# Optimization experiments

Hardware: AMD Instinct MI355X
Metric: run time of the kernel (lower is better)

## Reference

```python
import jax, jax.numpy as jnp
import numpy as np

N, C, H, W = 1024, 16, 32, 32
E = 4096


def setup_inputs() -> dict:
    key = jax.random.key(0)
    ks = jax.random.split(key, 10)
    feats = jax.random.normal(ks[0], (N, C, H, W), dtype=jnp.float32)
    src = jax.random.randint(ks[1], (E,), 0, N)
    dst = jax.random.randint(ks[2], (E,), 0, N)
    sign = jax.random.randint(ks[3], (E,), 0, 2) * 2 - 1  # values in {-1, +1}
    edges = jnp.stack([src, sign, dst], axis=1).astype(jnp.int64)
    s = 0.05
    w1 = jax.random.normal(ks[4], (2 * C, 3 * C, 3, 3), dtype=jnp.float32) * s
    b1 = jnp.zeros((2 * C,), dtype=jnp.float32)
    w2 = jax.random.normal(ks[5], (2 * C, 2 * C, 3, 3), dtype=jnp.float32) * s
    b2 = jnp.zeros((2 * C,), dtype=jnp.float32)
    w3 = jax.random.normal(ks[6], (C, 2 * C, 3, 3), dtype=jnp.float32) * s
    b3 = jnp.zeros((C,), dtype=jnp.float32)
    return {"feats": feats, "edges": edges, "w1": w1, "b1": b1,
            "w2": w2, "b2": b2, "w3": w3, "b3": b3}


def _pool_edges(edges, feats, positive):
    # Bidirectional gather + scatter_add over selected edges.
    # Mask-by-zero keeps shapes static (equivalent math to torch.where selection).
    sign = edges[:, 1]
    mask = (sign > 0) if positive else (sign < 0)
    w = mask.astype(feats.dtype)[:, None, None, None]
    src = edges[:, 0]
    dst = edges[:, 2]
    pooled = jnp.zeros_like(feats)
    pooled = pooled.at[dst].add(feats[src] * w)  # src -> dst
    pooled = pooled.at[src].add(feats[dst] * w)  # dst -> src
    return pooled


def _conv(x, w, b):
    y = jax.lax.conv_general_dilated(
        x, w, window_strides=(1, 1), padding=((1, 1), (1, 1)),
        dimension_numbers=("NCHW", "OIHW", "NCHW"))
    return y + b[None, :, None, None]


def _leaky(x):
    return jax.nn.leaky_relu(x, negative_slope=0.1)


def reference(feats, edges, w1, b1, w2, b2, w3, b3):
    pos = _pool_edges(edges, feats, positive=True)
    neg = _pool_edges(edges, feats, positive=False)
    x = jnp.concatenate([feats, pos, neg], axis=1)  # [N, 3C, H, W]
    x = _leaky(_conv(x, w1, b1))
    x = _leaky(_conv(x, w2, b2))
    x = _leaky(_conv(x, w3, b3))
    return x
```

## Files before the change

### kernel.cpp

```cpp
#include <hip/hip_runtime.h>


#define NIMG 1024
#define CHW  16384
#define NEDGE 4096
#define MAXD 64

#define ICP1 56
#define KP1  456
#define ICP2 40
#define KP2  296
#define XSZ (34*34*ICP1)
#define WSZ (32*KP1)

typedef __attribute__((ext_vector_type(8))) _Float16 half8;
typedef __attribute__((ext_vector_type(4))) _Float16 half4;
typedef __attribute__((ext_vector_type(4))) float float4v;

__device__ __forceinline__ float leaky(float x) { return x > 0.f ? x : 0.1f * x; }

__global__ __launch_bounds__(256) void build_adj(
    const int* __restrict__ edges, int* __restrict__ deg, int* __restrict__ adj)
{
    const int e = blockIdx.x * 256 + threadIdx.x;
    const bool is64 = (edges[1] == 0);
    int s, sg, d;
    if (is64) { s = edges[6*e]; sg = edges[6*e + 2]; d = edges[6*e + 4]; }
    else      { s = edges[3*e]; sg = edges[3*e + 1]; d = edges[3*e + 2]; }
    const int tag_d = (d << 1) | (int)(sg > 0);
    const int tag_s = (s << 1) | (int)(sg > 0);
    int i = atomicAdd(&deg[s], 1); if (i < MAXD) adj[(s << 6) + i] = tag_d;
    int j = atomicAdd(&deg[d], 1); if (j < MAXD) adj[(d << 6) + j] = tag_s;
}

__global__ __launch_bounds__(256) void transpose_kernel(
    const float* __restrict__ feats, _Float16* __restrict__ fcl)
{
    const int n = blockIdx.x, tid = threadIdx.x;
    const float* fb = feats + (size_t)n * CHW;
    _Float16*    ob = fcl   + (size_t)n * 1024 * 16;
    #pragma unroll
    for (int it = 0; it < 4; ++it) {
        int p = it*256 + tid;
        float t[16];
        #pragma unroll
        for (int c = 0; c < 16; ++c) t[c] = fb[(c << 10) + p];
        half8 v0, v1;
        #pragma unroll
        for (int c = 0; c < 8; ++c) { v0[c] = (_Float16)t[c]; v1[c] = (_Float16)t[c+8]; }
        *(half8*)(ob + p*16)     = v0;
        *(half8*)(ob + p*16 + 8) = v1;
    }
}

__global__ __launch_bounds__(1024, 4) void conv_kernel(
    const _Float16* __restrict__ fcl,
    const int* __restrict__ deg, const int* __restrict__ adj,
    const float* __restrict__ w1, const float* __restrict__ b1,
    const float* __restrict__ w2, const float* __restrict__ b2,
    const float* __restrict__ w3, const float* __restrict__ b3,
    float* __restrict__ out)
{
    __shared__ __align__(16) _Float16 Xs[XSZ];
    __shared__ __align__(16) _Float16 Ws[WSZ];
    const int n    = blockIdx.x;
    const int tid  = threadIdx.x;
    const int wave = tid >> 6;
    const int lane = tid & 63;
    const int col  = lane & 15;
    const int quad = lane >> 4;

    {
        const half8* fc = (const half8*)(fcl + (size_t)n * CHW);
        const int p = tid;
        const int base = (((p >> 5) + 1)*34 + (p & 31) + 1) * ICP1;
        *(half8*)(Xs + base)     = fc[2*p];
        *(half8*)(Xs + base + 8) = fc[2*p + 1];

        int m = deg[n]; if (m > MAXD) m = MAXD;
        const int* al = adj + (n << 6);
        float ap[16], an[16];
        #pragma unroll
        for (int c = 0; c < 16; ++c) { ap[c] = 0.f; an[c] = 0.f; }
        for (int i = 0; i < m; ++i) {
            const int v = al[i];
            const half8* fb = (const half8*)(fcl + (size_t)(v >> 1) * CHW);
            half8 x0 = fb[2*p], x1 = fb[2*p + 1];
            if (v & 1) {
                #pragma unroll
                for (int c = 0; c < 8; ++c) { ap[c] += (float)x0[c]; ap[c+8] += (float)x1[c]; }
            } else {
                #pragma unroll
                for (int c = 0; c < 8; ++c) { an[c] += (float)x0[c]; an[c+8] += (float)x1[c]; }
            }
        }
        half8 h0, h1, h2, h3;
        #pragma unroll
        for (int c = 0; c < 8; ++c) { h0[c] = (_Float16)ap[c]; h1[c] = (_Float16)ap[c+8];
                                      h2[c] = (_Float16)an[c]; h3[c] = (_Float16)an[c+8]; }
        *(half8*)(Xs + base + 16) = h0;
        *(half8*)(Xs + base + 24) = h1;
        *(half8*)(Xs + base + 32) = h2;
        *(half8*)(Xs + base + 40) = h3;

        for (int i = tid; i < 32*432; i += 1024) {
            int oc = i / 432, r = i - oc*432;
            int ic = r / 9,   tap = r - ic*9;
            Ws[oc*KP1 + tap*48 + ic] = (_Float16)w1[i];
        }
        if (tid < 132) {
            int hp, wp;
            if      (tid < 34)  { hp = 0;        wp = tid; }
            else if (tid < 68)  { hp = 33;       wp = tid - 34; }
            else if (tid < 100) { hp = tid - 67; wp = 0; }
            else                { hp = tid - 99; wp = 33; }
            int hb = (hp*34 + wp) * ICP1;
            #pragma unroll
            for (int t = 0; t < 6; ++t) *(half8*)(Xs + hb + t*8) = (half8)0;
        }
        if (tid >= 160 && tid < 192) {
            int wb = (tid - 160)*KP1 + 432;
            #pragma unroll
            for (int t = 0; t < 3; ++t) *(half8*)(Ws + wb + t*8) = (half8)0;
        }
    }
    __syncthreads();

    float4v acc[2][4];

    {
        #pragma unroll
        for (int m = 0; m < 2; ++m)
            #pragma unroll
            for (int j = 0; j < 4; ++j) acc[m][j] = (float4v){0.f,0.f,0.f,0.f};
        int pixb[4];
        #pragma unroll
        for (int j = 0; j < 4; ++j) {
            int p = wave*64 + j*16 + col;
            pixb[j] = ((p >> 5)*34 + (p & 31)) * ICP1;
        }
        const int abase = col * KP1 + quad * 8;
        #pragma unroll
        for (int ks = 0; ks < 14; ++ks) {
            int kq  = ks*32 + quad*8;
            int tap = kq / 48;
            int off = 0;
            if (tap < 9) {
                int ic0 = kq - tap*48;
                int dh = tap / 3, dw = tap - dh*3;
                off = (dh*34 + dw)*ICP1 + ic0;
            }
            half8 a0 = *(const half8*)(Ws + abase + ks*32);
            half8 a1 = *(const half8*)(Ws + 16*KP1 + abase + ks*32);
            #pragma unroll
            for (int j = 0; j < 4; ++j) {
                half8 b = *(const half8*)(Xs + pixb[j] + off);
                acc[0][j] = __builtin_amdgcn_mfma_f32_16x16x32_f16(a0, b, acc[0][j], 0, 0, 0);
                acc[1][j] = __builtin_amdgcn_mfma_f32_16x16x32_f16(a1, b, acc[1][j], 0, 0, 0);
            }
        }
    }
    __syncthreads();

    {
        if (tid < 132) {
            int hp, wp;
            if      (tid < 34)  { hp = 0;        wp = tid; }
            else if (tid < 68)  { hp = 33;       wp = tid - 34; }
            else if (tid < 100) { hp = tid - 67; wp = 0; }
            else                { hp = tid - 99; wp = 33; }
            int hb = (hp*34 + wp) * ICP2;
            #pragma unroll
            for (int t = 0; t < 4; ++t) *(half8*)(Xs + hb + t*8) = (half8)0;
        }
        float bv[2][4];
        #pragma unroll
        for (int m = 0; m < 2; ++m)
            #pragma unroll
            for (int r = 0; r < 4; ++r) bv[m][r] = b1[m*16 + quad*4 + r];
        #pragma unroll
        for (int m = 0; m < 2; ++m)
            #pragma unroll
            for (int j = 0; j < 4; ++j) {
                int p = wave*64 + j*16 + col;
                _Float16* y = Xs + ((((p>>5)+1)*34) + (p&31) + 1)*ICP2 + m*16 + quad*4;
                half4 v;
                #pragma unroll
                for (int r = 0; r < 4; ++r) v[r] = (_Float16)leaky(acc[m][j][r] + bv[m][r]);
                *(half4*)y = v;
            }
        for (int i = tid; i < 32*288; i += 1024) {
            int oc = i / 288, r = i - oc*288;
            int ic = r / 9,   tap = r - ic*9;
            Ws[oc*KP2 + tap*32 + ic] = (_Float16)w2[i];
        }
    }
    __syncthreads();

    {
        #pragma unroll
        for (int m = 0; m < 2; ++m)
            #pragma unroll
            for (int j = 0; j < 4; ++j) acc[m][j] = (float4v){0.f,0.f,0.f,0.f};
        int pixb[4];
        #pragma unroll
        for (int j = 0; j < 4; ++j) {
            int p = wave*64 + j*16 + col;
            pixb[j] = ((p >> 5)*34 + (p & 31)) * ICP2;
        }
        const int abase = col * KP2 + quad * 8;
        #pragma unroll
        for (int ks = 0; ks < 9; ++ks) {
            int kq  = ks*32 + quad*8;
            int tap = kq >> 5, ic0 = kq & 31;
            int dh = tap / 3, dw = tap - dh*3;
            int off = (dh*34 + dw)*ICP2 + ic0;
            half8 a0 = *(const half8*)(Ws + abase + ks*32);
            half8 a1 = *(const half8*)(Ws + 16*KP2 + abase + ks*32);
            #pragma unroll
            for (int j = 0; j < 4; ++j) {
                half8 b = *(const half8*)(Xs + pixb[j] + off);
                acc[0][j] = __builtin_amdgcn_mfma_f32_16x16x32_f16(a0, b, acc[0][j], 0, 0, 0);
                acc[1][j] = __builtin_amdgcn_mfma_f32_16x16x32_f16(a1, b, acc[1][j], 0, 0, 0);
            }
        }
    }
    __syncthreads();

    {
        float bv[2][4];
        #pragma unroll
        for (int m = 0; m < 2; ++m)
            #pragma unroll
            for (int r = 0; r < 4; ++r) bv[m][r] = b2[m*16 + quad*4 + r];
        #pragma unroll
        for (int m = 0; m < 2; ++m)
            #pragma unroll
            for (int j = 0; j < 4; ++j) {
                int p = wave*64 + j*16 + col;
                _Float16* y = Xs + ((((p>>5)+1)*34) + (p&31) + 1)*ICP2 + m*16 + quad*4;
                half4 v;
                #pragma unroll
                for (int r = 0; r < 4; ++r) v[r] = (_Float16)leaky(acc[m][j][r] + bv[m][r]);
                *(half4*)y = v;
            }
        for (int i = tid; i < 16*288; i += 1024) {
            int oc = i / 288, r = i - oc*288;
            int ic = r / 9,   tap = r - ic*9;
            Ws[oc*KP2 + tap*32 + ic] = (_Float16)w3[i];
        }
    }
    __syncthreads();

    {
        float4v a3[4];
        #pragma unroll
        for (int j = 0; j < 4; ++j) a3[j] = (float4v){0.f,0.f,0.f,0.f};
        int pixb[4];
        #pragma unroll
        for (int j = 0; j < 4; ++j) {
            int p = wave*64 + j*16 + col;
            pixb[j] = ((p >> 5)*34 + (p & 31)) * ICP2;
        }
        const int abase = col * KP2 + quad * 8;
        #pragma unroll
        for (int ks = 0; ks < 9; ++ks) {
            int kq  = ks*32 + quad*8;
            int tap = kq >> 5, ic0 = kq & 31;
            int dh = tap / 3, dw = tap - dh*3;
            int off = (dh*34 + dw)*ICP2 + ic0;
            half8 a0 = *(const half8*)(Ws + abase + ks*32);
            #pragma unroll
            for (int j = 0; j < 4; ++j) {
                half8 b = *(const half8*)(Xs + pixb[j] + off);
                a3[j] = __builtin_amdgcn_mfma_f32_16x16x32_f16(a0, b, a3[j], 0, 0, 0);
            }
        }
        float bv[4];
        #pragma unroll
        for (int r = 0; r < 4; ++r) bv[r] = b3[quad*4 + r];
        float* op = out + (size_t)n * CHW;
        #pragma unroll
        for (int j = 0; j < 4; ++j) {
            int p = wave*64 + j*16 + col;
            #pragma unroll
            for (int r = 0; r < 4; ++r)
                op[(quad*4 + r)*1024 + p] = leaky(a3[j][r] + bv[r]);
        }
    }
}

extern "C" void kernel_launch(void* const* d_in, const int* in_sizes, int n_in,
                              void* d_out, int out_size, void* d_ws, size_t ws_size,
                              hipStream_t stream) {
    const float* feats = (const float*)d_in[0];
    const int*   edges = (const int*)  d_in[1];
    const float* w1 = (const float*)d_in[2];
    const float* b1 = (const float*)d_in[3];
    const float* w2 = (const float*)d_in[4];
    const float* b2 = (const float*)d_in[5];
    const float* w3 = (const float*)d_in[6];
    const float* b3 = (const float*)d_in[7];
    float* out = (float*)d_out;

    _Float16* fcl = (_Float16*)d_ws;
    int* deg = (int*)((char*)d_ws + (32u << 20));
    int* adj = deg + NIMG;

    hipMemsetAsync(deg, 0, NIMG * sizeof(int), stream);
    build_adj<<<dim3(NEDGE/256), dim3(256), 0, stream>>>(edges, deg, adj);
    transpose_kernel<<<dim3(NIMG), dim3(256), 0, stream>>>(feats, fcl);
    conv_kernel<<<dim3(NIMG), dim3(1024), 0, stream>>>(fcl, deg, adj,
                                                       w1, b1, w2, b2, w3, b3, out);
}
```

Measured before the change: 251.6 us.

## Pre-pack fp16 conv weights once, vectorize transpose loads, unroll neighbor gather

Conv weights are converted to fp16 and packed into the padded per-tap layout once, inside the edge-building kernel, so each conv block can copy them into shared memory with 16-byte vector loads. This replaces the per-block scalar fp32 loads that used divisions and scattered stores. The transpose kernel now reads float4 vectors per channel. The neighbor aggregation loop is unrolled by four so that several gathers are in flight at once. The costs are extra workspace, more registers in the gather loop, and weight packing serialized into the small build_adj grid.

```diff
diff --git a/kernel.cpp b/kernel.cpp
--- a/kernel.cpp
+++ b/kernel.cpp
@@ -13,6 +13,11 @@
 #define XSZ (34*34*ICP1)
 #define WSZ (32*KP1)
 
+#define WG1N (32*KP1)
+#define WG2N (32*KP2)
+#define WG3N (16*KP2)
+#define WGTOT (WG1N+WG2N+WG3N)
+
 typedef __attribute__((ext_vector_type(8))) _Float16 half8;
 typedef __attribute__((ext_vector_type(4))) _Float16 half4;
 typedef __attribute__((ext_vector_type(4))) float float4v;
@@ -20,7 +25,9 @@
 __device__ __forceinline__ float leaky(float x) { return x > 0.f ? x : 0.1f * x; }
 
 __global__ __launch_bounds__(256) void build_adj(
-    const int* __restrict__ edges, int* __restrict__ deg, int* __restrict__ adj)
+    const int* __restrict__ edges, int* __restrict__ deg, int* __restrict__ adj,
+    const float* __restrict__ w1, const float* __restrict__ w2,
+    const float* __restrict__ w3, _Float16* __restrict__ wg)
 {
     const int e = blockIdx.x * 256 + threadIdx.x;
     const bool is64 = (edges[1] == 0);
@@ -31,6 +38,26 @@
     const int tag_s = (s << 1) | (int)(sg > 0);
     int i = atomicAdd(&deg[s], 1); if (i < MAXD) adj[(s << 6) + i] = tag_d;
     int j = atomicAdd(&deg[d], 1); if (j < MAXD) adj[(d << 6) + j] = tag_s;
+
+    for (int t = e; t < WGTOT; t += NEDGE) {
+        _Float16 val = (_Float16)0.f;
+        if (t < WG1N) {
+            int oc = t / KP1, r = t - oc * KP1;
+            if (r < 432) { int tap = r / 48, ic = r - tap * 48;
+                           val = (_Float16)w1[(oc*48 + ic)*9 + tap]; }
+        } else if (t < WG1N + WG2N) {
+            int u = t - WG1N;
+            int oc = u / KP2, r = u - oc * KP2;
+            if (r < 288) { int tap = r / 32, ic = r - tap * 32;
+                           val = (_Float16)w2[(oc*32 + ic)*9 + tap]; }
+        } else {
+            int u = t - (WG1N + WG2N);
+            int oc = u / KP2, r = u - oc * KP2;
+            if (r < 288) { int tap = r / 32, ic = r - tap * 32;
+                           val = (_Float16)w3[(oc*32 + ic)*9 + tap]; }
+        }
+        wg[t] = val;
+    }
 }
 
 __global__ __launch_bounds__(256) void transpose_kernel(
@@ -39,27 +66,26 @@
     const int n = blockIdx.x, tid = threadIdx.x;
     const float* fb = feats + (size_t)n * CHW;
     _Float16*    ob = fcl   + (size_t)n * 1024 * 16;
+    const int p0 = tid * 4;
+    float4v t[16];
     #pragma unroll
-    for (int it = 0; it < 4; ++it) {
-        int p = it*256 + tid;
-        float t[16];
-        #pragma unroll
-        for (int c = 0; c < 16; ++c) t[c] = fb[(c << 10) + p];
+    for (int c = 0; c < 16; ++c) t[c] = *(const float4v*)(fb + (c << 10) + p0);
+    #pragma unroll
+    for (int u = 0; u < 4; ++u) {
         half8 v0, v1;
         #pragma unroll
-        for (int c = 0; c < 8; ++c) { v0[c] = (_Float16)t[c]; v1[c] = (_Float16)t[c+8]; }
-        *(half8*)(ob + p*16)     = v0;
-        *(half8*)(ob + p*16 + 8) = v1;
+        for (int c = 0; c < 8; ++c) { v0[c] = (_Float16)t[c][u]; v1[c] = (_Float16)t[c+8][u]; }
+        *(half8*)(ob + (p0+u)*16)     = v0;
+        *(half8*)(ob + (p0+u)*16 + 8) = v1;
     }
 }
 
 __global__ __launch_bounds__(1024, 4) void conv_kernel(
     const _Float16* __restrict__ fcl,
     const int* __restrict__ deg, const int* __restrict__ adj,
-    const float* __restrict__ w1, const float* __restrict__ b1,
-    const float* __restrict__ w2, const float* __restrict__ b2,
-    const float* __restrict__ w3, const float* __restrict__ b3,
-    float* __restrict__ out)
+    const _Float16* __restrict__ wg,
+    const float* __restrict__ b1, const float* __restrict__ b2,
+    const float* __restrict__ b3, float* __restrict__ out)
 {
     __shared__ __align__(16) _Float16 Xs[XSZ];
     __shared__ __align__(16) _Float16 Ws[WSZ];
@@ -82,7 +108,27 @@
         float ap[16], an[16];
         #pragma unroll
         for (int c = 0; c < 16; ++c) { ap[c] = 0.f; an[c] = 0.f; }
-        for (int i = 0; i < m; ++i) {
+        int i = 0;
+        for (; i + 4 <= m; i += 4) {
+            int v0 = al[i], v1 = al[i+1], v2 = al[i+2], v3 = al[i+3];
+            const half8* f0 = (const half8*)(fcl + (size_t)(v0 >> 1) * CHW);
+            const half8* f1 = (const half8*)(fcl + (size_t)(v1 >> 1) * CHW);
+            const half8* f2 = (const half8*)(fcl + (size_t)(v2 >> 1) * CHW);
+            const half8* f3 = (const half8*)(fcl + (size_t)(v3 >> 1) * CHW);
+            half8 x00 = f0[2*p], x01 = f0[2*p+1];
+            half8 x10 = f1[2*p], x11 = f1[2*p+1];
+            half8 x20 = f2[2*p], x21 = f2[2*p+1];
+            half8 x30 = f3[2*p], x31 = f3[2*p+1];
+            if (v0 & 1) { for (int c = 0; c < 8; ++c) { ap[c] += (float)x00[c]; ap[c+8] += (float)x01[c]; } }
+            else        { for (int c = 0; c < 8; ++c) { an[c] += (float)x00[c]; an[c+8] += (float)x01[c]; } }
+            if (v1 & 1) { for (int c = 0; c < 8; ++c) { ap[c] += (float)x10[c]; ap[c+8] += (float)x11[c]; } }
+            else        { for (int c = 0; c < 8; ++c) { an[c] += (float)x10[c]; an[c+8] += (float)x11[c]; } }
+            if (v2 & 1) { for (int c = 0; c < 8; ++c) { ap[c] += (float)x20[c]; ap[c+8] += (float)x21[c]; } }
+            else        { for (int c = 0; c < 8; ++c) { an[c] += (float)x20[c]; an[c+8] += (float)x21[c]; } }
+            if (v3 & 1) { for (int c = 0; c < 8; ++c) { ap[c] += (float)x30[c]; ap[c+8] += (float)x31[c]; } }
+            else        { for (int c = 0; c < 8; ++c) { an[c] += (float)x30[c]; an[c+8] += (float)x31[c]; } }
+        }
+        for (; i < m; ++i) {
             const int v = al[i];
             const half8* fb = (const half8*)(fcl + (size_t)(v >> 1) * CHW);
             half8 x0 = fb[2*p], x1 = fb[2*p + 1];
@@ -103,10 +149,10 @@
         *(half8*)(Xs + base + 32) = h2;
         *(half8*)(Xs + base + 40) = h3;
 
-        for (int i = tid; i < 32*432; i += 1024) {
-            int oc = i / 432, r = i - oc*432;
-            int ic = r / 9,   tap = r - ic*9;
-            Ws[oc*KP1 + tap*48 + ic] = (_Float16)w1[i];
+        {
+            const half8* src = (const half8*)wg;
+            half8* dst = (half8*)Ws;
+            for (int t = tid; t < WG1N/8; t += 1024) dst[t] = src[t];
         }
         if (tid < 132) {
             int hp, wp;
@@ -117,11 +163,6 @@
             int hb = (hp*34 + wp) * ICP1;
             #pragma unroll
             for (int t = 0; t < 6; ++t) *(half8*)(Xs + hb + t*8) = (half8)0;
-        }
-        if (tid >= 160 && tid < 192) {
-            int wb = (tid - 160)*KP1 + 432;
-            #pragma unroll
-            for (int t = 0; t < 3; ++t) *(half8*)(Ws + wb + t*8) = (half8)0;
         }
     }
     __syncthreads();
@@ -189,10 +230,10 @@
                 for (int r = 0; r < 4; ++r) v[r] = (_Float16)leaky(acc[m][j][r] + bv[m][r]);
                 *(half4*)y = v;
             }
-        for (int i = tid; i < 32*288; i += 1024) {
-            int oc = i / 288, r = i - oc*288;
-            int ic = r / 9,   tap = r - ic*9;
-            Ws[oc*KP2 + tap*32 + ic] = (_Float16)w2[i];
+        {
+            const half8* src = (const half8*)(wg + WG1N);
+            half8* dst = (half8*)Ws;
+            for (int t = tid; t < WG2N/8; t += 1024) dst[t] = src[t];
         }
     }
     __syncthreads();
@@ -244,10 +285,10 @@
                 for (int r = 0; r < 4; ++r) v[r] = (_Float16)leaky(acc[m][j][r] + bv[m][r]);
                 *(half4*)y = v;
             }
-        for (int i = tid; i < 16*288; i += 1024) {
-            int oc = i / 288, r = i - oc*288;
-            int ic = r / 9,   tap = r - ic*9;
-            Ws[oc*KP2 + tap*32 + ic] = (_Float16)w3[i];
+        {
+            const half8* src = (const half8*)(wg + WG1N + WG2N);
+            half8* dst = (half8*)Ws;
+            for (int t = tid; t < WG3N/8; t += 1024) dst[t] = src[t];
         }
     }
     __syncthreads();
@@ -306,10 +347,11 @@
     _Float16* fcl = (_Float16*)d_ws;
     int* deg = (int*)((char*)d_ws + (32u << 20));
     int* adj = deg + NIMG;
+    _Float16* wg = (_Float16*)((char*)d_ws + (32u << 20) + 4096 + NIMG*MAXD*4);
 
     hipMemsetAsync(deg, 0, NIMG * sizeof(int), stream);
-    build_adj<<<dim3(NEDGE/256), dim3(256), 0, stream>>>(edges, deg, adj);
+    build_adj<<<dim3(NEDGE/256), dim3(256), 0, stream>>>(edges, deg, adj, w1, w2, w3, wg);
     transpose_kernel<<<dim3(NIMG), dim3(256), 0, stream>>>(feats, fcl);
-    conv_kernel<<<dim3(NIMG), dim3(1024), 0, stream>>>(fcl, deg, adj,
-                                                       w1, b1, w2, b2, w3, b3, out);
+    conv_kernel<<<dim3(NIMG), dim3(1024), 0, stream>>>(fcl, deg, adj, wg,
+                                                       b1, b2, b3, out);
 }
```

After: 233.3 us. 7.3% less time.
